# Kernel tuning notes

Measured on AMD Instinct MI355X. Metric: run time of the kernel, lower is better.

The kernel has to match this reference:

```python
import jax, jax.numpy as jnp
import numpy as np


def setup_inputs() -> dict:
    key = jax.random.key(0)
    ks = jax.random.split(key, 7)
    H, O, B, T = 256, 128, 2048, 100
    s = 1.0 / np.sqrt(H)
    return {
        "C": jax.random.normal(ks[0], (B, H), dtype=jnp.float32),
        "W_ih": jax.random.uniform(ks[1], (4 * H, H), jnp.float32, -s, s),
        "W_hh": jax.random.uniform(ks[2], (4 * H, H), jnp.float32, -s, s),
        "b_ih": jax.random.uniform(ks[3], (4 * H,), jnp.float32, -s, s),
        "b_hh": jax.random.uniform(ks[4], (4 * H,), jnp.float32, -s, s),
        "W_out": jax.random.uniform(ks[5], (O, H), jnp.float32, -s, s),
        "b_out": jax.random.uniform(ks[6], (O,), jnp.float32, -s, s),
        "max_seq_len": T,
    }


def reference(C, W_ih, W_hh, b_ih, b_hh, W_out, b_out, max_seq_len):
    B, H = C.shape
    # Input contribution is the same at every step (the module re-feeds C).
    x_gates = C @ W_ih.T + b_ih + b_hh  # [B, 4H]

    def step(carry, _):
        h, c = carry
        gates = x_gates + h @ W_hh.T  # [B, 4H]
        i, f, g, o = jnp.split(gates, 4, axis=-1)  # torch gate order: i,f,g,o
        c_new = jax.nn.sigmoid(f) * c + jax.nn.sigmoid(i) * jnp.tanh(g)
        h_new = jax.nn.sigmoid(o) * jnp.tanh(c_new)
        y = h_new @ W_out.T + b_out  # [B, O]
        return (h_new, c_new), y

    init = (jnp.zeros((B, H), C.dtype), jnp.zeros((B, H), C.dtype))
    _, ys = jax.lax.scan(step, init, None, length=max_seq_len)
    return ys  # [T, B, O]
```

## Files before the change

### kernel.cpp

```cpp
#include <hip/hip_runtime.h>
#include <hip/hip_bf16.h>

typedef __attribute__((ext_vector_type(8))) short  bf16x8;
typedef __attribute__((ext_vector_type(4))) short  s16x4;
typedef __attribute__((ext_vector_type(4))) float  f32x4;

#define LOG2E 1.44269504088896340736f

template<int N> struct ic { static constexpr int v = N; };

__device__ __forceinline__ unsigned short f2bf(float x) {
    union { float f; unsigned int u; } v; v.f = x;
    unsigned int u = v.u;
    u += 0x7fffu + ((u >> 16) & 1u);
    return (unsigned short)(u >> 16);
}

__device__ __forceinline__ float fast_sigmoid(float x) {
    float e = __builtin_amdgcn_exp2f(-LOG2E * x);
    return __builtin_amdgcn_rcpf(1.0f + e);
}
__device__ __forceinline__ float fast_tanh(float x) {
    float e = __builtin_amdgcn_exp2f(2.0f * LOG2E * x);
    return 1.0f - 2.0f * __builtin_amdgcn_rcpf(1.0f + e);
}

__global__ void pack_w_big(const float* __restrict__ W, unsigned short* __restrict__ dst) {
    int idx  = blockIdx.x * 256 + threadIdx.x;
    int lane = idx & 63;
    int fid  = idx >> 6;
    int j    = fid & 7;
    int kk   = (fid >> 3) & 7;
    int w    = fid >> 6;
    int g    = j >> 1, tn = j & 1;
    int R    = g * 256 + w * 32 + tn * 16 + (lane & 15);
    int kb   = kk * 32 + 4 * (lane >> 4);
    const float* src = W + (size_t)R * 256 + kb;
    union { unsigned short s[8]; uint4 v; } u;
#pragma unroll
    for (int e = 0; e < 8; ++e) {
        int k = (e & 3) + 16 * (e >> 2);
        u.s[e] = f2bf(src[k]);
    }
    *(uint4*)(dst + (size_t)idx * 8) = u.v;
}

__global__ void pack_w_out(const float* __restrict__ W, unsigned short* __restrict__ dst) {
    int idx  = blockIdx.x * 256 + threadIdx.x;
    int lane = idx & 63;
    int fid  = idx >> 6;
    int kk   = fid & 7;
    int wv   = fid >> 3;
    int R    = wv * 16 + (lane & 15);
    int kb   = kk * 32 + 4 * (lane >> 4);
    const float* src = W + (size_t)R * 256 + kb;
    union { unsigned short s[8]; uint4 v; } u;
#pragma unroll
    for (int e = 0; e < 8; ++e) {
        int k = (e & 3) + 16 * (e >> 2);
        u.s[e] = f2bf(src[k]);
    }
    *(uint4*)(dst + (size_t)idx * 8) = u.v;
}

__global__ __launch_bounds__(512, 2) void lstm_main(
    const float* __restrict__ C,
    const unsigned short* __restrict__ Wih_p,
    const unsigned short* __restrict__ Whh_p,
    const unsigned short* __restrict__ Wout_p,
    const float* __restrict__ b_ih,
    const float* __restrict__ b_hh,
    const float* __restrict__ b_out,
    float* __restrict__ Y,
    int T, int Btot)
{
    __shared__ short hbuf[2][16 * 256];
    __shared__ short wpark[8][8192];

    const int tid  = threadIdx.x;
    const int l    = tid & 63;
    const int wid  = tid >> 6;
    const int l15  = l & 15;
    const int g4   = l >> 4;
    const int row0 = blockIdx.x * 16;

    const unsigned short* wib = Wih_p + (size_t)wid * 32768;
    const unsigned short* whb = Whh_p + (size_t)wid * 32768;

    {
        int r  = tid >> 5;
        int cb = tid & 31;
        const float* src = C + (size_t)(row0 + r) * 256 + cb * 8;
        float4 f0 = *(const float4*)(src);
        float4 f1 = *(const float4*)(src + 4);
        int m  = 9 * (r & 7);
        int s0 = cb * 2;
        short* hb = hbuf[0] + r * 256;
        union { unsigned short s[4]; unsigned long long v; } p0, p1;
        p0.s[0] = f2bf(f0.x); p0.s[1] = f2bf(f0.y); p0.s[2] = f2bf(f0.z); p0.s[3] = f2bf(f0.w);
        p1.s[0] = f2bf(f1.x); p1.s[1] = f2bf(f1.y); p1.s[2] = f2bf(f1.z); p1.s[3] = f2bf(f1.w);
        *(unsigned long long*)(hb + ((s0 ^ m) * 4))       = p0.v;
        *(unsigned long long*)(hb + (((s0 + 1) ^ m) * 4)) = p1.v;
    }

    {
        bf16x8 tmp[16];
#pragma unroll
        for (int f = 0; f < 16; ++f)
            tmp[f] = *(const bf16x8*)(whb + ((size_t)f * 64 + l) * 8);
#pragma unroll
        for (int f = 0; f < 16; ++f)
            *(bf16x8*)&wpark[wid][(f * 64 + l) * 8] = tmp[f];
    }
    __syncthreads();

    const int msw = 9 * (l15 & 7);
    auto loadA = [&](const short* buf, int kk) -> bf16x8 {
        int slo = kk * 8 + g4;
        const short* base = buf + l15 * 256;
        s16x4 lo = *(const s16x4*)(base + ((slo ^ msw) * 4));
        s16x4 hi = *(const s16x4*)(base + (((slo + 4) ^ msw) * 4));
        bf16x8 a;
        a[0] = lo[0]; a[1] = lo[1]; a[2] = lo[2]; a[3] = lo[3];
        a[4] = hi[0]; a[5] = hi[1]; a[6] = hi[2]; a[7] = hi[3];
        return a;
    };
    auto loadB = [&](const unsigned short* wb, int kk, int j) -> bf16x8 {
        return *(const bf16x8*)(wb + (((size_t)kk * 8 + j) * 64 + l) * 8);
    };

    bf16x8 wout[8];
#pragma unroll
    for (int kk = 0; kk < 8; ++kk)
        wout[kk] = *(const bf16x8*)(Wout_p + ((size_t)(wid * 8 + kk) * 64 + l) * 8);

    f32x4 acc[8];
    f32x4 accy;
    bf16x8 b0[8], b1[8];

#pragma unroll
    for (int j = 0; j < 8; ++j) b0[j] = loadB(wib, 0, j);
#pragma unroll
    for (int j = 0; j < 8; ++j) b1[j] = loadB(wib, 1, j);

#pragma unroll
    for (int j = 0; j < 8; ++j) acc[j] = (f32x4){0.f, 0.f, 0.f, 0.f};

    auto xg_kk = [&](auto kkc, bf16x8 (&bb)[8], const unsigned short* nwb, auto nxtc) {
        constexpr int kk = decltype(kkc)::v;
        constexpr int nx = decltype(nxtc)::v;
        bf16x8 a = loadA(hbuf[0], kk);
#pragma unroll
        for (int j = 0; j < 8; ++j)
            acc[j] = __builtin_amdgcn_mfma_f32_16x16x32_bf16(a, bb[j], acc[j], 0, 0, 0);
#pragma unroll
        for (int j = 0; j < 8; ++j) bb[j] = loadB(nwb, nx, j);
    };
    xg_kk(ic<0>{}, b0, wib, ic<2>{});
    xg_kk(ic<1>{}, b1, wib, ic<3>{});
    xg_kk(ic<2>{}, b0, wib, ic<4>{});
    xg_kk(ic<3>{}, b1, wib, ic<5>{});
    xg_kk(ic<4>{}, b0, wib, ic<6>{});
    xg_kk(ic<5>{}, b1, wib, ic<7>{});
    xg_kk(ic<6>{}, b0, whb, ic<2>{});
    xg_kk(ic<7>{}, b1, whb, ic<3>{});

    f32x4 xg[8];
#pragma unroll
    for (int j = 0; j < 8; ++j) {
        int g = j >> 1, tn = j & 1;
        int col = g * 256 + wid * 32 + tn * 16 + l15;
        xg[j] = acc[j] + (b_ih[col] + b_hh[col]);
    }

    float cst[8];
#pragma unroll
    for (int i = 0; i < 8; ++i) cst[i] = 0.f;
    const float by = b_out[wid * 16 + l15];

    auto update_write = [&](short* nxtb) {
#pragma unroll
        for (int tn = 0; tn < 2; ++tn) {
#pragma unroll
            for (int r = 0; r < 4; ++r) {
                float iv = fast_sigmoid(acc[0 + tn][r]);
                float fv = fast_sigmoid(acc[2 + tn][r]);
                float gv = fast_tanh(acc[4 + tn][r]);
                float ov = fast_sigmoid(acc[6 + tn][r]);
                float cn = fv * cst[tn * 4 + r] + iv * gv;
                cst[tn * 4 + r] = cn;
                float hn = ov * fast_tanh(cn);
                int row = 4 * g4 + r;
                int col = wid * 32 + tn * 16 + l15;
                int ps  = (col >> 2) ^ (9 * (row & 7));
                nxtb[row * 256 + ps * 4 + (col & 3)] = (short)f2bf(hn);
            }
        }
    };

#pragma unroll
    for (int j = 0; j < 8; ++j) acc[j] = xg[j];
    update_write(hbuf[1]);
    __syncthreads();

    auto step_parked = [&](const short* curb, auto kkc) {
        constexpr int kk = decltype(kkc)::v;
        bf16x8 a = loadA(curb, kk);
        accy = __builtin_amdgcn_mfma_f32_16x16x32_bf16(a, wout[kk], accy, 0, 0, 0);
#pragma unroll
        for (int j = 0; j < 8; ++j) {
            bf16x8 b = *(const bf16x8*)&wpark[wid][((kk * 8 + j) * 64 + l) * 8];
            acc[j] = __builtin_amdgcn_mfma_f32_16x16x32_bf16(a, b, acc[j], 0, 0, 0);
        }
    };
    auto step_stream = [&](const short* curb, auto kkc, bf16x8 (&bb)[8], auto nxtc) {
        constexpr int kk = decltype(kkc)::v;
        constexpr int nx = decltype(nxtc)::v;
        bf16x8 a = loadA(curb, kk);
        accy = __builtin_amdgcn_mfma_f32_16x16x32_bf16(a, wout[kk], accy, 0, 0, 0);
#pragma unroll
        for (int j = 0; j < 8; ++j)
            acc[j] = __builtin_amdgcn_mfma_f32_16x16x32_bf16(a, bb[j], acc[j], 0, 0, 0);
#pragma unroll
        for (int j = 0; j < 8; ++j) bb[j] = loadB(whb, nx, j);
    };

    for (int t = 1; t < T; ++t) {
        const short* curb = hbuf[t & 1];
        short*       nxtb = hbuf[(t + 1) & 1];
        accy = (f32x4){by, by, by, by};
#pragma unroll
        for (int j = 0; j < 8; ++j) acc[j] = xg[j];

        step_parked(curb, ic<0>{});
        step_parked(curb, ic<1>{});
        step_stream(curb, ic<2>{}, b0, ic<4>{});
        step_stream(curb, ic<3>{}, b1, ic<5>{});
        step_stream(curb, ic<4>{}, b0, ic<6>{});
        step_stream(curb, ic<5>{}, b1, ic<7>{});
        step_stream(curb, ic<6>{}, b0, ic<2>{});
        step_stream(curb, ic<7>{}, b1, ic<3>{});

        {
            float* yp = Y + ((size_t)(t - 1) * Btot + row0 + 4 * g4) * 128 + wid * 16 + l15;
#pragma unroll
            for (int r = 0; r < 4; ++r)
                __builtin_nontemporal_store(accy[r], yp + (size_t)r * 128);
        }
        update_write(nxtb);
        __syncthreads();
    }

    {
        const short* curb = hbuf[T & 1];
        accy = (f32x4){by, by, by, by};
#pragma unroll
        for (int kk = 0; kk < 8; ++kk) {
            bf16x8 a = loadA(curb, kk);
            accy = __builtin_amdgcn_mfma_f32_16x16x32_bf16(a, wout[kk], accy, 0, 0, 0);
        }
        float* yp = Y + ((size_t)(T - 1) * Btot + row0 + 4 * g4) * 128 + wid * 16 + l15;
#pragma unroll
        for (int r = 0; r < 4; ++r)
            __builtin_nontemporal_store(accy[r], yp + (size_t)r * 128);
    }
}

extern "C" void kernel_launch(void* const* d_in, const int* in_sizes, int n_in,
                              void* d_out, int out_size, void* d_ws, size_t ws_size,
                              hipStream_t stream) {
    const float* C     = (const float*)d_in[0];
    const float* W_ih  = (const float*)d_in[1];
    const float* W_hh  = (const float*)d_in[2];
    const float* b_ih  = (const float*)d_in[3];
    const float* b_hh  = (const float*)d_in[4];
    const float* W_out = (const float*)d_in[5];
    const float* b_out = (const float*)d_in[6];

    const int H    = 256;
    const int Btot = in_sizes[0] / H;
    const int O    = in_sizes[5] / H;
    const int T    = out_size / (Btot * O);

    unsigned short* Whh_p  = (unsigned short*)d_ws;
    unsigned short* Wih_p  = Whh_p + (1 << 18);
    unsigned short* Wout_p = Wih_p + (1 << 18);

    hipLaunchKernelGGL(pack_w_big, dim3(128), dim3(256), 0, stream, W_hh, Whh_p);
    hipLaunchKernelGGL(pack_w_big, dim3(128), dim3(256), 0, stream, W_ih, Wih_p);
    hipLaunchKernelGGL(pack_w_out, dim3(16),  dim3(256), 0, stream, W_out, Wout_p);
    hipLaunchKernelGGL(lstm_main, dim3(Btot / 16), dim3(512), 0, stream,
                       C, Wih_p, Whh_p, Wout_p, b_ih, b_hh, b_out,
                       (float*)d_out, T, Btot);
}
```

Baseline: 743.1 us.

## Keep two more W_hh k-slices in registers and stagger k-order across blocks

Two additional W_hh k-slices (k=2,3) now stay resident in registers, so only k=4..7 are streamed from global memory at each step instead of k=2..7. Each block also starts its k-loop at a rotated offset chosen from its block index, which spreads the weight-streaming load across blocks so they do not all hit the same slices at the same moment. The bias initialisation is folded into the first MFMA of each step. The cost is 16 more bf16x8 registers per lane, which can lower occupancy or cause spills, plus four instantiated copies of the time loop, which grows code size.

```diff
diff --git a/kernel.cpp b/kernel.cpp
--- a/kernel.cpp
+++ b/kernel.cpp
@@ -142,28 +142,28 @@
     for (int j = 0; j < 8; ++j) b0[j] = loadB(wib, 0, j);
 #pragma unroll
     for (int j = 0; j < 8; ++j) b1[j] = loadB(wib, 1, j);
-
 #pragma unroll
     for (int j = 0; j < 8; ++j) acc[j] = (f32x4){0.f, 0.f, 0.f, 0.f};
 
-    auto xg_kk = [&](auto kkc, bf16x8 (&bb)[8], const unsigned short* nwb, auto nxtc) {
+    auto xg_kk = [&](auto kkc) {
         constexpr int kk = decltype(kkc)::v;
-        constexpr int nx = decltype(nxtc)::v;
         bf16x8 a = loadA(hbuf[0], kk);
 #pragma unroll
-        for (int j = 0; j < 8; ++j)
-            acc[j] = __builtin_amdgcn_mfma_f32_16x16x32_bf16(a, bb[j], acc[j], 0, 0, 0);
-#pragma unroll
-        for (int j = 0; j < 8; ++j) bb[j] = loadB(nwb, nx, j);
-    };
-    xg_kk(ic<0>{}, b0, wib, ic<2>{});
-    xg_kk(ic<1>{}, b1, wib, ic<3>{});
-    xg_kk(ic<2>{}, b0, wib, ic<4>{});
-    xg_kk(ic<3>{}, b1, wib, ic<5>{});
-    xg_kk(ic<4>{}, b0, wib, ic<6>{});
-    xg_kk(ic<5>{}, b1, wib, ic<7>{});
-    xg_kk(ic<6>{}, b0, whb, ic<2>{});
-    xg_kk(ic<7>{}, b1, whb, ic<3>{});
+        for (int j = 0; j < 8; ++j) {
+            bf16x8 b;
+            if constexpr (kk & 1) b = b1[j]; else b = b0[j];
+            acc[j] = __builtin_amdgcn_mfma_f32_16x16x32_bf16(a, b, acc[j], 0, 0, 0);
+        }
+        if constexpr (kk < 6) {
+#pragma unroll
+            for (int j = 0; j < 8; ++j) {
+                if constexpr (kk & 1) b1[j] = loadB(wib, kk + 2, j);
+                else                  b0[j] = loadB(wib, kk + 2, j);
+            }
+        }
+    };
+    xg_kk(ic<0>{}); xg_kk(ic<1>{}); xg_kk(ic<2>{}); xg_kk(ic<3>{});
+    xg_kk(ic<4>{}); xg_kk(ic<5>{}); xg_kk(ic<6>{}); xg_kk(ic<7>{});
 
     f32x4 xg[8];
 #pragma unroll
@@ -172,6 +172,12 @@
         int col = g * 256 + wid * 32 + tn * 16 + l15;
         xg[j] = acc[j] + (b_ih[col] + b_hh[col]);
     }
+
+    bf16x8 r2[8], r3[8];
+#pragma unroll
+    for (int j = 0; j < 8; ++j) r2[j] = loadB(whb, 2, j);
+#pragma unroll
+    for (int j = 0; j < 8; ++j) r3[j] = loadB(whb, 3, j);
 
     float cst[8];
 #pragma unroll
@@ -203,53 +209,77 @@
     update_write(hbuf[1]);
     __syncthreads();
 
-    auto step_parked = [&](const short* curb, auto kkc) {
-        constexpr int kk = decltype(kkc)::v;
-        bf16x8 a = loadA(curb, kk);
-        accy = __builtin_amdgcn_mfma_f32_16x16x32_bf16(a, wout[kk], accy, 0, 0, 0);
-#pragma unroll
-        for (int j = 0; j < 8; ++j) {
-            bf16x8 b = *(const bf16x8*)&wpark[wid][((kk * 8 + j) * 64 + l) * 8];
-            acc[j] = __builtin_amdgcn_mfma_f32_16x16x32_bf16(a, b, acc[j], 0, 0, 0);
-        }
-    };
-    auto step_stream = [&](const short* curb, auto kkc, bf16x8 (&bb)[8], auto nxtc) {
-        constexpr int kk = decltype(kkc)::v;
-        constexpr int nx = decltype(nxtc)::v;
-        bf16x8 a = loadA(curb, kk);
-        accy = __builtin_amdgcn_mfma_f32_16x16x32_bf16(a, wout[kk], accy, 0, 0, 0);
-#pragma unroll
-        for (int j = 0; j < 8; ++j)
-            acc[j] = __builtin_amdgcn_mfma_f32_16x16x32_bf16(a, bb[j], acc[j], 0, 0, 0);
-#pragma unroll
-        for (int j = 0; j < 8; ++j) bb[j] = loadB(whb, nx, j);
-    };
-
-    for (int t = 1; t < T; ++t) {
-        const short* curb = hbuf[t & 1];
-        short*       nxtb = hbuf[(t + 1) & 1];
-        accy = (f32x4){by, by, by, by};
-#pragma unroll
-        for (int j = 0; j < 8; ++j) acc[j] = xg[j];
-
-        step_parked(curb, ic<0>{});
-        step_parked(curb, ic<1>{});
-        step_stream(curb, ic<2>{}, b0, ic<4>{});
-        step_stream(curb, ic<3>{}, b1, ic<5>{});
-        step_stream(curb, ic<4>{}, b0, ic<6>{});
-        step_stream(curb, ic<5>{}, b1, ic<7>{});
-        step_stream(curb, ic<6>{}, b0, ic<2>{});
-        step_stream(curb, ic<7>{}, b1, ic<3>{});
-
-        {
-            float* yp = Y + ((size_t)(t - 1) * Btot + row0 + 4 * g4) * 128 + wid * 16 + l15;
-#pragma unroll
-            for (int r = 0; r < 4; ++r)
-                __builtin_nontemporal_store(accy[r], yp + (size_t)r * 128);
-        }
-        update_write(nxtb);
-        __syncthreads();
-    }
+    auto run = [&](auto Sc) {
+        constexpr int S = decltype(Sc)::v;
+        constexpr int k0 = S & 7, k1 = (S + 1) & 7;
+        if constexpr (k0 >= 4) {
+#pragma unroll
+            for (int j = 0; j < 8; ++j) {
+                if constexpr (k0 & 1) b1[j] = loadB(whb, k0, j);
+                else                  b0[j] = loadB(whb, k0, j);
+            }
+        }
+        if constexpr (k1 >= 4) {
+#pragma unroll
+            for (int j = 0; j < 8; ++j) {
+                if constexpr (k1 & 1) b1[j] = loadB(whb, k1, j);
+                else                  b0[j] = loadB(whb, k1, j);
+            }
+        }
+        for (int t = 1; t < T; ++t) {
+            const short* curb = hbuf[t & 1];
+            short*       nxtb = hbuf[(t + 1) & 1];
+
+            auto phase = [&](auto pc) {
+                constexpr int p = decltype(pc)::v;
+                constexpr int k = (S + p) & 7;
+                bf16x8 a = loadA(curb, k);
+                if constexpr (p == 0)
+                    accy = __builtin_amdgcn_mfma_f32_16x16x32_bf16(
+                        a, wout[k], (f32x4){by, by, by, by}, 0, 0, 0);
+                else
+                    accy = __builtin_amdgcn_mfma_f32_16x16x32_bf16(a, wout[k], accy, 0, 0, 0);
+#pragma unroll
+                for (int j = 0; j < 8; ++j) {
+                    bf16x8 b;
+                    if constexpr (k < 2)       b = *(const bf16x8*)&wpark[wid][((k * 8 + j) * 64 + l) * 8];
+                    else if constexpr (k == 2) b = r2[j];
+                    else if constexpr (k == 3) b = r3[j];
+                    else if constexpr (k & 1)  b = b1[j];
+                    else                       b = b0[j];
+                    if constexpr (p == 0)
+                        acc[j] = __builtin_amdgcn_mfma_f32_16x16x32_bf16(a, b, xg[j], 0, 0, 0);
+                    else
+                        acc[j] = __builtin_amdgcn_mfma_f32_16x16x32_bf16(a, b, acc[j], 0, 0, 0);
+                }
+                constexpr int kn = (S + p + 2) & 7;
+                if constexpr (kn >= 4) {
+#pragma unroll
+                    for (int j = 0; j < 8; ++j) {
+                        if constexpr (kn & 1) b1[j] = loadB(whb, kn, j);
+                        else                  b0[j] = loadB(whb, kn, j);
+                    }
+                }
+            };
+            phase(ic<0>{}); phase(ic<1>{}); phase(ic<2>{}); phase(ic<3>{});
+            phase(ic<4>{}); phase(ic<5>{}); phase(ic<6>{}); phase(ic<7>{});
+
+            {
+                float* yp = Y + ((size_t)(t - 1) * Btot + row0 + 4 * g4) * 128 + wid * 16 + l15;
+#pragma unroll
+                for (int r = 0; r < 4; ++r)
+                    __builtin_nontemporal_store(accy[r], yp + (size_t)r * 128);
+            }
+            update_write(nxtb);
+            __syncthreads();
+        }
+    };
+
+    const int sv = (blockIdx.x >> 3) & 3;
+    if      (sv == 0) run(ic<0>{});
+    else if (sv == 1) run(ic<2>{});
+    else if (sv == 2) run(ic<4>{});
+    else              run(ic<6>{});
 
     {
         const short* curb = hbuf[T & 1];
```

Measured after the change: 800.9 us. 1.08x slower.
